# Optimization experiments

Hardware: AMD Instinct MI355X
Metric: run time of the kernel (lower is better)

The kernel has to match this reference:

```python
import jax, jax.numpy as jnp
import numpy as np

LATENT = 256


def setup_inputs() -> dict:
    key = jax.random.key(0)
    ks = jax.random.split(key, 10)
    B, T, V, E, D0, H, L = 512, 200, 3356, 1128, 20000, 1024, LATENT

    def glorot(k, shape):
        fan_out, fan_in = shape
        std = np.sqrt(2.0 / (fan_in + fan_out)).astype(np.float32)
        return jax.random.normal(k, shape, dtype=jnp.float32) * std

    x = jax.random.uniform(ks[0], (B, D0), dtype=jnp.float32)
    item_ids = jax.random.randint(ks[1], (B, T), 0, V, dtype=jnp.int32)
    embed = jax.random.normal(ks[2], (V, E), dtype=jnp.float32)
    Wi = glorot(ks[3], (L, E))
    bi = jnp.zeros((L,), jnp.float32)
    We1 = glorot(ks[4], (H, D0))
    be1 = jnp.zeros((H,), jnp.float32)
    We2 = glorot(ks[5], (2 * L, H))
    be2 = jnp.zeros((2 * L,), jnp.float32)
    Wd1 = glorot(ks[6], (H, L))
    bd1 = jnp.zeros((H,), jnp.float32)
    Wd2 = glorot(ks[7], (D0, H))
    bd2 = jnp.zeros((D0,), jnp.float32)
    # dropout(p=0.5) mask, pre-scaled by 1/(1-p)=2
    drop_mask = (jax.random.bernoulli(ks[8], 0.5, (B, D0))).astype(jnp.float32) * 2.0
    eps = jax.random.normal(ks[9], (B, L), dtype=jnp.float32)
    return {"x": x, "item_ids": item_ids, "embed": embed, "Wi": Wi, "bi": bi,
            "We1": We1, "be1": be1, "We2": We2, "be2": be2,
            "Wd1": Wd1, "bd1": bd1, "Wd2": Wd2, "bd2": bd2,
            "drop_mask": drop_mask, "eps": eps}


def reference(x, item_ids, embed, Wi, bi, We1, be1, We2, be2,
              Wd1, bd1, Wd2, bd2, drop_mask, eps):
    # item feature path: embedding lookup -> linear -> per-sequence stats
    item = jnp.einsum('bte,le->btl', embed[item_ids], Wi) + bi        # [B,T,L]
    mean = jnp.mean(item, axis=1)                                      # [B,L]
    deviation = jnp.std(item, axis=1, ddof=1)                          # torch.std (unbiased)

    # encoder: F.normalize (L2 over features) -> dropout -> tanh MLP
    xn = x / jnp.maximum(jnp.linalg.norm(x, axis=1, keepdims=True), 1e-12)
    h = xn * drop_mask
    h = jnp.tanh(h @ We1.T + be1)
    gparams = h @ We2.T + be2                                          # [B,2L]
    mu, logvar = gparams[:, :LATENT], gparams[:, LATENT:]

    # reparam: MVN with diagonal covariance diag(deviation) == mean + sqrt(dev)*eps
    prior = mean + jnp.sqrt(deviation) * eps
    z = prior * jnp.exp(0.5 * logvar) + mu

    # decoder: tanh MLP
    hd = jnp.tanh(z @ Wd1.T + bd1)
    recon_x = hd @ Wd2.T + bd2                                         # [B,D0]
    return recon_x, mu, logvar
```

## Files before the change

kernel.cpp:

```cpp
#include <hip/hip_runtime.h>
#include <hip/hip_bf16.h>

typedef __bf16 bf16x8 __attribute__((ext_vector_type(8)));
typedef float f32x4 __attribute__((ext_vector_type(4)));
typedef unsigned short u16x8 __attribute__((ext_vector_type(8)));

static __device__ __forceinline__ unsigned short f2bf(float f){
  unsigned int u = __float_as_uint(f);
  u += 0x7fffu + ((u >> 16) & 1u);
  return (unsigned short)(u >> 16);
}

static __device__ __forceinline__ u16x8 cvt8(const float4& a, const float4& b){
  u16x8 r;
  r[0]=f2bf(a.x); r[1]=f2bf(a.y); r[2]=f2bf(a.z); r[3]=f2bf(a.w);
  r[4]=f2bf(b.x); r[5]=f2bf(b.y); r[6]=f2bf(b.z); r[7]=f2bf(b.w);
  return r;
}

static __device__ __forceinline__ void gload16(const void* g, void* l){
  __builtin_amdgcn_global_load_lds(
      (const __attribute__((address_space(1))) unsigned int*)g,
      (__attribute__((address_space(3))) unsigned int*)l, 16, 0, 0);
}

template<int EPI>
__global__ __launch_bounds__(256, 2) void gemm_big(
    const unsigned short* __restrict__ A, const unsigned short* __restrict__ Bw,
    const float* __restrict__ bias,
    float* __restrict__ Cf, unsigned short* __restrict__ Cbf,
    int M, int N, int K, int kchunk)
{
  constexpr int BK = 32;
  constexpr int AE = 128 * BK;
  constexpr int BE = 256 * BK;
  constexpr int BUFE = AE + BE;
  __shared__ unsigned short lds[3 * BUFE];

  const int tid  = threadIdx.x, lane = tid & 63, wave = tid >> 6;
  const int bm0  = blockIdx.y * 128, bn0 = blockIdx.x * 256;
  const int k0   = blockIdx.z * kchunk;
  const int kend = min(K, k0 + kchunk);
  const int nk   = (kend - k0) / BK;
  const int fr = lane & 15, fq = lane >> 4;
  const int wn = wave * 64;

  const int srow = lane >> 2, scol = (lane & 3) * 8;

  auto stage = [&](int buf, int t){
    char* base = (char*)(lds + buf * BUFE);
    const int kk = k0 + t * BK;
    #pragma unroll
    for (int c = 0; c < 2; c++) {
      const int ch = 2 * wave + c;
      const int r = min(bm0 + ch * 16 + srow, M - 1);
      gload16(A + (size_t)r * K + kk + scol, base + ch * 1024);
    }
    #pragma unroll
    for (int c = 0; c < 4; c++) {
      const int ch = 4 * wave + c;
      const int r = min(bn0 + ch * 16 + srow, N - 1);
      gload16(Bw + (size_t)r * K + kk + scol, base + 8192 + ch * 1024);
    }
  };

  stage(0, 0);
  if (nk > 1) stage(1, 1);

  f32x4 acc[8][4] = {};
  int cur = 0;

  for (int t = 0; t < nk; ++t) {
    if (t < nk - 1) asm volatile("s_waitcnt vmcnt(6)" ::: "memory");
    else            asm volatile("s_waitcnt vmcnt(0)" ::: "memory");
    __builtin_amdgcn_s_barrier();
    __builtin_amdgcn_sched_barrier(0);

    if (t + 2 < nk) {
      const int sb = (cur >= 1) ? cur - 1 : cur + 2;
      stage(sb, t + 2);
    }

    const unsigned short* lA = lds + cur * BUFE;
    const unsigned short* lB = lA + AE;
    u16x8 af[8], bg[4];
    #pragma unroll
    for (int i = 0; i < 8; i++) af[i] = *(const u16x8*)&lA[(i*16 + fr) * BK + fq * 8];
    #pragma unroll
    for (int j = 0; j < 4; j++) bg[j] = *(const u16x8*)&lB[(wn + j*16 + fr) * BK + fq * 8];
    #pragma unroll
    for (int j = 0; j < 4; j++)
      #pragma unroll
      for (int i = 0; i < 8; i++)
        acc[i][j] = __builtin_amdgcn_mfma_f32_16x16x32_bf16(
            __builtin_bit_cast(bf16x8, af[i]),
            __builtin_bit_cast(bf16x8, bg[j]),
            acc[i][j], 0, 0, 0);
    asm volatile("s_waitcnt lgkmcnt(0)" ::: "memory");
    __builtin_amdgcn_sched_barrier(0);
    __builtin_amdgcn_s_barrier();
    cur = (cur == 2) ? 0 : cur + 1;
  }

  #pragma unroll
  for (int i = 0; i < 8; i++)
    #pragma unroll
    for (int j = 0; j < 4; j++)
      #pragma unroll
      for (int r = 0; r < 4; r++) {
        int row = bm0 + i*16 + fq*4 + r;
        int col = bn0 + wn + j*16 + fr;
        if (row < M && col < N) {
          float v = acc[i][j][r];
          if constexpr (EPI == 0) {
            Cf[(size_t)row * N + col] = v + (bias ? bias[col] : 0.0f);
          } else if constexpr (EPI == 1) {
            atomicAdd(&Cf[(size_t)row * N + col], v);
          } else {
            Cbf[(size_t)row * N + col] = f2bf(tanhf(v + bias[col]));
          }
        }
      }
}

template<int EPI>
__global__ __launch_bounds__(256) void gemm_sm(
    const unsigned short* __restrict__ A, const unsigned short* __restrict__ Bw,
    const float* __restrict__ bias,
    float* __restrict__ Cf, unsigned short* __restrict__ Cbf,
    int M, int N, int K, int kchunk)
{
  constexpr int BM = 128, BN = 128, BK = 32;
  __shared__ unsigned short lds[(BM + BN) * BK];
  unsigned short* lA = lds;
  unsigned short* lB = lds + BM * BK;

  const int tid  = threadIdx.x, lane = tid & 63, wave = tid >> 6;
  const int bm0  = blockIdx.y * BM, bn0 = blockIdx.x * BN;
  const int k0   = blockIdx.z * kchunk;
  const int kend = min(K, k0 + kchunk);
  const int fr = lane & 15, fq = lane >> 4;
  const int wm = (wave >> 1) * 64, wn = (wave & 1) * 64;

  const bool isA  = wave < 2;
  const int cbase = (wave & 1) * 4;
  const int srow  = lane >> 2, scol = (lane & 3) * 8;
  const unsigned short* G = isA ? A : Bw;
  const int glim = (isA ? M : N) - 1;
  const int g0   = isA ? bm0 : bn0;
  unsigned short* ldst = isA ? lA : lB;

  f32x4 acc[4][4] = {};

  for (int kk = k0; kk < kend; kk += BK) {
    #pragma unroll
    for (int c = 0; c < 4; c++) {
      const int ch = cbase + c;
      const int r = min(g0 + ch * 16 + srow, glim);
      gload16(G + (size_t)r * K + kk + scol, (char*)ldst + ch * 1024);
    }
    __syncthreads();
    u16x8 af[4], bg[4];
    #pragma unroll
    for (int i = 0; i < 4; i++) af[i] = *(const u16x8*)&lA[(wm + i*16 + fr) * BK + fq * 8];
    #pragma unroll
    for (int j = 0; j < 4; j++) bg[j] = *(const u16x8*)&lB[(wn + j*16 + fr) * BK + fq * 8];
    #pragma unroll
    for (int i = 0; i < 4; i++)
      #pragma unroll
      for (int j = 0; j < 4; j++)
        acc[i][j] = __builtin_amdgcn_mfma_f32_16x16x32_bf16(
            __builtin_bit_cast(bf16x8, af[i]),
            __builtin_bit_cast(bf16x8, bg[j]),
            acc[i][j], 0, 0, 0);
    __syncthreads();
  }

  #pragma unroll
  for (int i = 0; i < 4; i++)
    #pragma unroll
    for (int j = 0; j < 4; j++)
      #pragma unroll
      for (int r = 0; r < 4; r++) {
        int row = bm0 + wm + i*16 + fq*4 + r;
        int col = bn0 + wn + j*16 + fr;
        if (row < M && col < N) {
          float v = acc[i][j][r];
          if constexpr (EPI == 0) {
            Cf[(size_t)row * N + col] = v + (bias ? bias[col] : 0.0f);
          } else if constexpr (EPI == 1) {
            atomicAdd(&Cf[(size_t)row * N + col], v);
          } else {
            Cbf[(size_t)row * N + col] = f2bf(tanhf(v + bias[col]));
          }
        }
      }
}

__global__ __launch_bounds__(256) void cvt4_kernel(
    const float* __restrict__ s0, unsigned short* __restrict__ d0, int n0,
    const float* __restrict__ s1, unsigned short* __restrict__ d1, int n1,
    const float* __restrict__ s2, unsigned short* __restrict__ d2, int n2,
    const float* __restrict__ s3, unsigned short* __restrict__ d3, int n3)
{
  int i = (blockIdx.x * 256 + threadIdx.x) * 8;
  const float* s; unsigned short* d;
  if (i < n0)            { s = s0; d = d0; }
  else if ((i -= n0) < n1) { s = s1; d = d1; }
  else if ((i -= n1) < n2) { s = s2; d = d2; }
  else if ((i -= n2) < n3) { s = s3; d = d3; }
  else return;
  const float4* q = (const float4*)(s + i);
  *(u16x8*)(d + i) = cvt8(q[0], q[1]);
}

__global__ __launch_bounds__(256) void cvtpad_kernel(
    const float* __restrict__ src, unsigned short* __restrict__ dst,
    int rows, int scols, int dcols)
{
  int i8 = blockIdx.x * 256 + threadIdx.x;
  int c8 = dcols / 8;
  if (i8 >= rows * c8) return;
  int r = i8 / c8, c0 = (i8 % c8) * 8;
  const float* s = src + (size_t)r * scols;
  u16x8 o;
  #pragma unroll
  for (int e = 0; e < 8; e++) { int c = c0 + e; o[e] = (c < scols) ? f2bf(s[c]) : (unsigned short)0; }
  *(u16x8*)(dst + (size_t)r * dcols + c0) = o;
}

__global__ __launch_bounds__(256) void ynorm_kernel(
    const float* __restrict__ x, const float* __restrict__ dm,
    unsigned short* __restrict__ y, float* __restrict__ ninv, int D0)
{
  const int b = blockIdx.x, tid = threadIdx.x;
  const float4* x4 = (const float4*)(x + (size_t)b * D0);
  const float4* d4 = (const float4*)(dm + (size_t)b * D0);
  ushort4* y4 = (ushort4*)(y + (size_t)b * D0);
  const int n4 = D0 / 4;
  float ss = 0.f;
  for (int i = tid; i < n4; i += 256) {
    float4 xv = x4[i], dv = d4[i];
    ss += xv.x*xv.x + xv.y*xv.y + xv.z*xv.z + xv.w*xv.w;
    ushort4 o;
    o.x = f2bf(xv.x*dv.x); o.y = f2bf(xv.y*dv.y);
    o.z = f2bf(xv.z*dv.z); o.w = f2bf(xv.w*dv.w);
    y4[i] = o;
  }
  #pragma unroll
  for (int off = 32; off > 0; off >>= 1) ss += __shfl_down(ss, off);
  __shared__ float wsum[4];
  if ((tid & 63) == 0) wsum[tid >> 6] = ss;
  __syncthreads();
  if (tid == 0) {
    float t = wsum[0] + wsum[1] + wsum[2] + wsum[3];
    ninv[b] = 1.0f / fmaxf(sqrtf(t), 1e-12f);
  }
}

__global__ __launch_bounds__(256) void stats_kernel(
    const float* __restrict__ proj, const int* __restrict__ ids,
    const float* __restrict__ bi, const float* __restrict__ eps,
    float* __restrict__ prior, int T)
{
  const int b = blockIdx.x, l = threadIdx.x;
  __shared__ int sid[256];
  if (l < T) sid[l] = ids[b * T + l];
  __syncthreads();
  float s1 = 0.f, s2 = 0.f;
  #pragma unroll 4
  for (int t = 0; t < T; t++) {
    float p = proj[(size_t)sid[t] * 256 + l];
    s1 += p; s2 += p * p;
  }
  float var = fmaxf((s2 - s1 * s1 / (float)T) / (float)(T - 1), 0.f);
  float dev = sqrtf(var);
  float mean = s1 / (float)T + bi[l];
  prior[b * 256 + l] = mean + sqrtf(dev) * eps[b * 256 + l];
}

__global__ __launch_bounds__(256) void epi1_kernel(
    const float* __restrict__ C1, const float* __restrict__ ninv,
    const float* __restrict__ be1, unsigned short* __restrict__ h)
{
  int i = blockIdx.x * 256 + threadIdx.x;
  int b = i >> 10, n = i & 1023;
  h[i] = f2bf(tanhf(ninv[b] * C1[i] + be1[n]));
}

__global__ __launch_bounds__(256) void z_kernel(
    const float* __restrict__ gp, const float* __restrict__ prior,
    const float* __restrict__ be2,
    float* __restrict__ out_mu, float* __restrict__ out_lv,
    unsigned short* __restrict__ z)
{
  int i = blockIdx.x * 256 + threadIdx.x;
  int b = i >> 8, l = i & 255;
  float mu = gp[b * 512 + l]       + be2[l];
  float lv = gp[b * 512 + 256 + l] + be2[256 + l];
  out_mu[i] = mu;
  out_lv[i] = lv;
  z[i] = f2bf(prior[i] * expf(0.5f * lv) + mu);
}

extern "C" void kernel_launch(void* const* d_in, const int* in_sizes, int n_in,
                              void* d_out, int out_size, void* d_ws, size_t ws_size,
                              hipStream_t stream)
{
  const float* x     = (const float*)d_in[0];
  const int*   ids   = (const int*)  d_in[1];
  const float* embed = (const float*)d_in[2];
  const float* Wi    = (const float*)d_in[3];
  const float* bi    = (const float*)d_in[4];
  const float* We1   = (const float*)d_in[5];
  const float* be1   = (const float*)d_in[6];
  const float* We2   = (const float*)d_in[7];
  const float* be2   = (const float*)d_in[8];
  const float* Wd1   = (const float*)d_in[9];
  const float* bd1   = (const float*)d_in[10];
  const float* Wd2   = (const float*)d_in[11];
  const float* bd2   = (const float*)d_in[12];
  const float* dm    = (const float*)d_in[13];
  const float* eps   = (const float*)d_in[14];

  constexpr int B = 512, T = 200, V = 3356, E = 1128, Ep = 1152, D0 = 20000, H = 1024, L = 256;

  char* w = (char*)d_ws;
  auto carve = [&](size_t bytes) { char* p = w; w += (bytes + 255) & ~(size_t)255; return p; };
  unsigned short* We1b  = (unsigned short*)carve((size_t)H * D0 * 2);
  unsigned short* Wd2b  = (unsigned short*)carve((size_t)D0 * H * 2);
  unsigned short* We2b  = (unsigned short*)carve((size_t)2 * L * H * 2);
  unsigned short* Wd1b  = (unsigned short*)carve((size_t)H * L * 2);
  unsigned short* embedb= (unsigned short*)carve((size_t)V * Ep * 2);
  unsigned short* Wib   = (unsigned short*)carve((size_t)L * Ep * 2);
  float*          proj  = (float*)         carve((size_t)V * L * 4);
  unsigned short* y     = (unsigned short*)carve((size_t)B * D0 * 2);
  float*          C1    = (float*)         carve((size_t)B * H * 4);
  unsigned short* h     = (unsigned short*)carve((size_t)B * H * 2);
  float*          gp    = (float*)         carve((size_t)B * 2 * L * 4);
  float*          prior = (float*)         carve((size_t)B * L * 4);
  unsigned short* z     = (unsigned short*)carve((size_t)B * L * 2);
  unsigned short* hd    = (unsigned short*)carve((size_t)B * H * 2);
  float*          ninv  = (float*)         carve((size_t)B * 4);

  float* out_recon = (float*)d_out;
  float* out_mu    = out_recon + (size_t)B * D0;
  float* out_lv    = out_mu + (size_t)B * L;

  {
    const int n0 = H * D0, n1 = D0 * H, n2 = 2 * L * H, n3 = H * L;
    const int nblk = (n0 + n1 + n2 + n3) / (8 * 256);
    cvt4_kernel<<<nblk, 256, 0, stream>>>(We1, We1b, n0, Wd2, Wd2b, n1,
                                          We2, We2b, n2, Wd1, Wd1b, n3);
  }
  cvtpad_kernel<<<(V * (Ep/8) + 255) / 256, 256, 0, stream>>>(embed, embedb, V, E, Ep);
  cvtpad_kernel<<<(L * (Ep/8) + 255) / 256, 256, 0, stream>>>(Wi, Wib, L, E, Ep);

  ynorm_kernel<<<B, 256, 0, stream>>>(x, dm, y, ninv, D0);

  hipMemsetAsync(proj, 0, (size_t)V * L * 4, stream);
  gemm_sm<1><<<dim3(2, 27, 4), 256, 0, stream>>>(
      embedb, Wib, nullptr, proj, nullptr, V, L, Ep, 288);
  stats_kernel<<<B, 256, 0, stream>>>(proj, ids, bi, eps, prior, T);

  hipMemsetAsync(C1, 0, (size_t)B * H * 4, stream);
  gemm_big<1><<<dim3(4, 4, 32), 256, 0, stream>>>(
      y, We1b, nullptr, C1, nullptr, B, H, D0, 640);
  epi1_kernel<<<(B * H) / 256, 256, 0, stream>>>(C1, ninv, be1, h);

  hipMemsetAsync(gp, 0, (size_t)B * 2 * L * 4, stream);
  gemm_sm<1><<<dim3(4, 4, 4), 256, 0, stream>>>(
      h, We2b, nullptr, gp, nullptr, B, 2 * L, H, 256);
  z_kernel<<<(B * L) / 256, 256, 0, stream>>>(gp, prior, be2, out_mu, out_lv, z);

  gemm_sm<2><<<dim3(8, 4, 1), 256, 0, stream>>>(
      z, Wd1b, bd1, nullptr, hd, B, H, L, 256);
  gemm_big<0><<<dim3(79, 4, 1), 256, 0, stream>>>(
      hd, Wd2b, bd2, out_recon, nullptr, B, D0, H, 1024);
}
```

Baseline: 296.7 us.

## Read fp32 weights directly in big GEMMs, converting to bf16 in-kernel

The separate pre-conversion pass that turned the two large weight matrices (We1, Wd2) into bf16 copies is removed. The big GEMM now stages fp32 weight tiles into LDS with an XOR swizzle and converts them to bf16 with packed convert instructions before the MFMAs. The tile also shrinks to 128x128 with a 3-deep prefetch, and the grid and split-K are retuned. This cuts a full read and write of about 80MB of weights, but doubles LDS traffic for B and adds conversion ALU work in the inner loop.

```diff
diff --git a/kernel.cpp b/kernel.cpp
--- a/kernel.cpp
+++ b/kernel.cpp
@@ -4,11 +4,18 @@
 typedef __bf16 bf16x8 __attribute__((ext_vector_type(8)));
 typedef float f32x4 __attribute__((ext_vector_type(4)));
 typedef unsigned short u16x8 __attribute__((ext_vector_type(8)));
+typedef unsigned int u32x4 __attribute__((ext_vector_type(4)));
 
 static __device__ __forceinline__ unsigned short f2bf(float f){
   unsigned int u = __float_as_uint(f);
   u += 0x7fffu + ((u >> 16) & 1u);
   return (unsigned short)(u >> 16);
+}
+
+static __device__ __forceinline__ unsigned int cvtpk(float lo, float hi){
+  unsigned int r;
+  asm("v_cvt_pk_bf16_f32 %0, %1, %2" : "=v"(r) : "v"(lo), "v"(hi));
+  return r;
 }
 
 static __device__ __forceinline__ u16x8 cvt8(const float4& a, const float4& b){
@@ -25,146 +32,78 @@
 }
 
 template<int EPI>
-__global__ __launch_bounds__(256, 2) void gemm_big(
-    const unsigned short* __restrict__ A, const unsigned short* __restrict__ Bw,
+__global__ __launch_bounds__(256, 2) void gemm_bigf(
+    const unsigned short* __restrict__ A, const float* __restrict__ Bw,
     const float* __restrict__ bias,
     float* __restrict__ Cf, unsigned short* __restrict__ Cbf,
     int M, int N, int K, int kchunk)
 {
-  constexpr int BK = 32;
-  constexpr int AE = 128 * BK;
-  constexpr int BE = 256 * BK;
-  constexpr int BUFE = AE + BE;
-  __shared__ unsigned short lds[3 * BUFE];
+  constexpr int BK = 32, BUFB = 8192 + 16384;
+  __shared__ char smem[3 * BUFB];
 
   const int tid  = threadIdx.x, lane = tid & 63, wave = tid >> 6;
-  const int bm0  = blockIdx.y * 128, bn0 = blockIdx.x * 256;
+  const int bm0  = blockIdx.y * 128, bn0 = blockIdx.x * 128;
   const int k0   = blockIdx.z * kchunk;
   const int kend = min(K, k0 + kchunk);
   const int nk   = (kend - k0) / BK;
   const int fr = lane & 15, fq = lane >> 4;
-  const int wn = wave * 64;
-
-  const int srow = lane >> 2, scol = (lane & 3) * 8;
+  const int wm = (wave >> 1) * 64, wn = (wave & 1) * 64;
+
+  const int ar_off = wave * 16 + (lane >> 2), ac_off = (lane & 3) * 8;
+  const int br_off = wave * 8 + (lane >> 3);
+  const int bg_off = (((lane & 7) ^ (lane >> 3)) << 2);
 
   auto stage = [&](int buf, int t){
-    char* base = (char*)(lds + buf * BUFE);
+    char* base = smem + buf * BUFB;
     const int kk = k0 + t * BK;
     #pragma unroll
     for (int c = 0; c < 2; c++) {
-      const int ch = 2 * wave + c;
-      const int r = min(bm0 + ch * 16 + srow, M - 1);
-      gload16(A + (size_t)r * K + kk + scol, base + ch * 1024);
+      const int r = min(bm0 + c * 64 + ar_off, M - 1);
+      gload16(A + (size_t)r * K + kk + ac_off, base + c * 4096 + wave * 1024);
     }
     #pragma unroll
     for (int c = 0; c < 4; c++) {
-      const int ch = 4 * wave + c;
-      const int r = min(bn0 + ch * 16 + srow, N - 1);
-      gload16(Bw + (size_t)r * K + kk + scol, base + 8192 + ch * 1024);
+      const int r = min(bn0 + c * 32 + br_off, N - 1);
+      gload16(Bw + (size_t)r * K + kk + bg_off, base + 8192 + c * 4096 + wave * 1024);
     }
   };
 
   stage(0, 0);
   if (nk > 1) stage(1, 1);
-
-  f32x4 acc[8][4] = {};
+  if (nk > 2) stage(2, 2);
+
+  f32x4 acc[4][4] = {};
   int cur = 0;
 
   for (int t = 0; t < nk; ++t) {
-    if (t < nk - 1) asm volatile("s_waitcnt vmcnt(6)" ::: "memory");
-    else            asm volatile("s_waitcnt vmcnt(0)" ::: "memory");
+    const int rem = nk - t - 1;
+    if (rem >= 2)      asm volatile("s_waitcnt vmcnt(12)" ::: "memory");
+    else if (rem == 1) asm volatile("s_waitcnt vmcnt(6)"  ::: "memory");
+    else               asm volatile("s_waitcnt vmcnt(0)"  ::: "memory");
     __builtin_amdgcn_s_barrier();
     __builtin_amdgcn_sched_barrier(0);
 
-    if (t + 2 < nk) {
-      const int sb = (cur >= 1) ? cur - 1 : cur + 2;
-      stage(sb, t + 2);
+    const unsigned short* lA = (const unsigned short*)(smem + cur * BUFB);
+    const char*           lB = smem + cur * BUFB + 8192;
+    u16x8 af[4], bg[4];
+    #pragma unroll
+    for (int i = 0; i < 4; i++) af[i] = *(const u16x8*)&lA[(wm + i*16 + fr) * BK + fq * 8];
+    #pragma unroll
+    for (int j = 0; j < 4; j++) {
+      const int r  = wn + j*16 + fr;
+      const int s0 = (((fq << 1) ^ (r & 7)) << 4);
+      const char* bp = lB + r * 128;
+      f32x4 u = *(const f32x4*)(bp + s0);
+      f32x4 v = *(const f32x4*)(bp + (s0 ^ 16));
+      u32x4 wv; wv[0]=cvtpk(u[0],u[1]); wv[1]=cvtpk(u[2],u[3]);
+                wv[2]=cvtpk(v[0],v[1]); wv[3]=cvtpk(v[2],v[3]);
+      bg[j] = __builtin_bit_cast(u16x8, wv);
     }
-
-    const unsigned short* lA = lds + cur * BUFE;
-    const unsigned short* lB = lA + AE;
-    u16x8 af[8], bg[4];
-    #pragma unroll
-    for (int i = 0; i < 8; i++) af[i] = *(const u16x8*)&lA[(i*16 + fr) * BK + fq * 8];
-    #pragma unroll
-    for (int j = 0; j < 4; j++) bg[j] = *(const u16x8*)&lB[(wn + j*16 + fr) * BK + fq * 8];
-    #pragma unroll
-    for (int j = 0; j < 4; j++)
-      #pragma unroll
-      for (int i = 0; i < 8; i++)
-        acc[i][j] = __builtin_amdgcn_mfma_f32_16x16x32_bf16(
-            __builtin_bit_cast(bf16x8, af[i]),
-            __builtin_bit_cast(bf16x8, bg[j]),
-            acc[i][j], 0, 0, 0);
     asm volatile("s_waitcnt lgkmcnt(0)" ::: "memory");
     __builtin_amdgcn_sched_barrier(0);
     __builtin_amdgcn_s_barrier();
-    cur = (cur == 2) ? 0 : cur + 1;
-  }
-
-  #pragma unroll
-  for (int i = 0; i < 8; i++)
-    #pragma unroll
-    for (int j = 0; j < 4; j++)
-      #pragma unroll
-      for (int r = 0; r < 4; r++) {
-        int row = bm0 + i*16 + fq*4 + r;
-        int col = bn0 + wn + j*16 + fr;
-        if (row < M && col < N) {
-          float v = acc[i][j][r];
-          if constexpr (EPI == 0) {
-            Cf[(size_t)row * N + col] = v + (bias ? bias[col] : 0.0f);
-          } else if constexpr (EPI == 1) {
-            atomicAdd(&Cf[(size_t)row * N + col], v);
-          } else {
-            Cbf[(size_t)row * N + col] = f2bf(tanhf(v + bias[col]));
-          }
-        }
-      }
-}
-
-template<int EPI>
-__global__ __launch_bounds__(256) void gemm_sm(
-    const unsigned short* __restrict__ A, const unsigned short* __restrict__ Bw,
-    const float* __restrict__ bias,
-    float* __restrict__ Cf, unsigned short* __restrict__ Cbf,
-    int M, int N, int K, int kchunk)
-{
-  constexpr int BM = 128, BN = 128, BK = 32;
-  __shared__ unsigned short lds[(BM + BN) * BK];
-  unsigned short* lA = lds;
-  unsigned short* lB = lds + BM * BK;
-
-  const int tid  = threadIdx.x, lane = tid & 63, wave = tid >> 6;
-  const int bm0  = blockIdx.y * BM, bn0 = blockIdx.x * BN;
-  const int k0   = blockIdx.z * kchunk;
-  const int kend = min(K, k0 + kchunk);
-  const int fr = lane & 15, fq = lane >> 4;
-  const int wm = (wave >> 1) * 64, wn = (wave & 1) * 64;
-
-  const bool isA  = wave < 2;
-  const int cbase = (wave & 1) * 4;
-  const int srow  = lane >> 2, scol = (lane & 3) * 8;
-  const unsigned short* G = isA ? A : Bw;
-  const int glim = (isA ? M : N) - 1;
-  const int g0   = isA ? bm0 : bn0;
-  unsigned short* ldst = isA ? lA : lB;
-
-  f32x4 acc[4][4] = {};
-
-  for (int kk = k0; kk < kend; kk += BK) {
-    #pragma unroll
-    for (int c = 0; c < 4; c++) {
-      const int ch = cbase + c;
-      const int r = min(g0 + ch * 16 + srow, glim);
-      gload16(G + (size_t)r * K + kk + scol, (char*)ldst + ch * 1024);
-    }
-    __syncthreads();
-    u16x8 af[4], bg[4];
-    #pragma unroll
-    for (int i = 0; i < 4; i++) af[i] = *(const u16x8*)&lA[(wm + i*16 + fr) * BK + fq * 8];
-    #pragma unroll
-    for (int j = 0; j < 4; j++) bg[j] = *(const u16x8*)&lB[(wn + j*16 + fr) * BK + fq * 8];
+    if (t + 3 < nk) stage(cur, t + 3);
+
     #pragma unroll
     for (int i = 0; i < 4; i++)
       #pragma unroll
@@ -173,7 +112,7 @@
             __builtin_bit_cast(bf16x8, af[i]),
             __builtin_bit_cast(bf16x8, bg[j]),
             acc[i][j], 0, 0, 0);
-    __syncthreads();
+    cur = (cur == 2) ? 0 : cur + 1;
   }
 
   #pragma unroll
@@ -197,6 +136,80 @@
       }
 }
 
+template<int EPI>
+__global__ __launch_bounds__(256) void gemm_sm(
+    const unsigned short* __restrict__ A, const unsigned short* __restrict__ Bw,
+    const float* __restrict__ bias,
+    float* __restrict__ Cf, unsigned short* __restrict__ Cbf,
+    int M, int N, int K, int kchunk)
+{
+  constexpr int BM = 128, BN = 128, BK = 32;
+  __shared__ unsigned short lds[(BM + BN) * BK];
+  unsigned short* lA = lds;
+  unsigned short* lB = lds + BM * BK;
+
+  const int tid  = threadIdx.x, lane = tid & 63, wave = tid >> 6;
+  const int bm0  = blockIdx.y * BM, bn0 = blockIdx.x * BN;
+  const int k0   = blockIdx.z * kchunk;
+  const int kend = min(K, k0 + kchunk);
+  const int fr = lane & 15, fq = lane >> 4;
+  const int wm = (wave >> 1) * 64, wn = (wave & 1) * 64;
+
+  const bool isA  = wave < 2;
+  const int cbase = (wave & 1) * 4;
+  const int srow  = lane >> 2, scol = (lane & 3) * 8;
+  const unsigned short* G = isA ? A : Bw;
+  const int glim = (isA ? M : N) - 1;
+  const int g0   = isA ? bm0 : bn0;
+  unsigned short* ldst = isA ? lA : lB;
+
+  f32x4 acc[4][4] = {};
+
+  for (int kk = k0; kk < kend; kk += BK) {
+    #pragma unroll
+    for (int c = 0; c < 4; c++) {
+      const int ch = cbase + c;
+      const int r = min(g0 + ch * 16 + srow, glim);
+      gload16(G + (size_t)r * K + kk + scol, (char*)ldst + ch * 1024);
+    }
+    __syncthreads();
+    u16x8 af[4], bg[4];
+    #pragma unroll
+    for (int i = 0; i < 4; i++) af[i] = *(const u16x8*)&lA[(wm + i*16 + fr) * BK + fq * 8];
+    #pragma unroll
+    for (int j = 0; j < 4; j++) bg[j] = *(const u16x8*)&lB[(wn + j*16 + fr) * BK + fq * 8];
+    #pragma unroll
+    for (int i = 0; i < 4; i++)
+      #pragma unroll
+      for (int j = 0; j < 4; j++)
+        acc[i][j] = __builtin_amdgcn_mfma_f32_16x16x32_bf16(
+            __builtin_bit_cast(bf16x8, af[i]),
+            __builtin_bit_cast(bf16x8, bg[j]),
+            acc[i][j], 0, 0, 0);
+    __syncthreads();
+  }
+
+  #pragma unroll
+  for (int i = 0; i < 4; i++)
+    #pragma unroll
+    for (int j = 0; j < 4; j++)
+      #pragma unroll
+      for (int r = 0; r < 4; r++) {
+        int row = bm0 + wm + i*16 + fq*4 + r;
+        int col = bn0 + wn + j*16 + fr;
+        if (row < M && col < N) {
+          float v = acc[i][j][r];
+          if constexpr (EPI == 0) {
+            Cf[(size_t)row * N + col] = v + (bias ? bias[col] : 0.0f);
+          } else if constexpr (EPI == 1) {
+            atomicAdd(&Cf[(size_t)row * N + col], v);
+          } else {
+            Cbf[(size_t)row * N + col] = f2bf(tanhf(v + bias[col]));
+          }
+        }
+      }
+}
+
 __global__ __launch_bounds__(256) void cvt4_kernel(
     const float* __restrict__ s0, unsigned short* __restrict__ d0, int n0,
     const float* __restrict__ s1, unsigned short* __restrict__ d1, int n1,
@@ -327,8 +340,6 @@
 
   char* w = (char*)d_ws;
   auto carve = [&](size_t bytes) { char* p = w; w += (bytes + 255) & ~(size_t)255; return p; };
-  unsigned short* We1b  = (unsigned short*)carve((size_t)H * D0 * 2);
-  unsigned short* Wd2b  = (unsigned short*)carve((size_t)D0 * H * 2);
   unsigned short* We2b  = (unsigned short*)carve((size_t)2 * L * H * 2);
   unsigned short* Wd1b  = (unsigned short*)carve((size_t)H * L * 2);
   unsigned short* embedb= (unsigned short*)carve((size_t)V * Ep * 2);
@@ -348,10 +359,9 @@
   float* out_lv    = out_mu + (size_t)B * L;
 
   {
-    const int n0 = H * D0, n1 = D0 * H, n2 = 2 * L * H, n3 = H * L;
-    const int nblk = (n0 + n1 + n2 + n3) / (8 * 256);
-    cvt4_kernel<<<nblk, 256, 0, stream>>>(We1, We1b, n0, Wd2, Wd2b, n1,
-                                          We2, We2b, n2, Wd1, Wd1b, n3);
+    const int n0 = 2 * L * H, n1 = H * L;
+    cvt4_kernel<<<(n0 + n1) / (8 * 256), 256, 0, stream>>>(
+        We2, We2b, n0, Wd1, Wd1b, n1, We2, We2b, 0, We2, We2b, 0);
   }
   cvtpad_kernel<<<(V * (Ep/8) + 255) / 256, 256, 0, stream>>>(embed, embedb, V, E, Ep);
   cvtpad_kernel<<<(L * (Ep/8) + 255) / 256, 256, 0, stream>>>(Wi, Wib, L, E, Ep);
@@ -364,8 +374,8 @@
   stats_kernel<<<B, 256, 0, stream>>>(proj, ids, bi, eps, prior, T);
 
   hipMemsetAsync(C1, 0, (size_t)B * H * 4, stream);
-  gemm_big<1><<<dim3(4, 4, 32), 256, 0, stream>>>(
-      y, We1b, nullptr, C1, nullptr, B, H, D0, 640);
+  gemm_bigf<1><<<dim3(8, 4, 25), 256, 0, stream>>>(
+      y, We1, nullptr, C1, nullptr, B, H, D0, 800);
   epi1_kernel<<<(B * H) / 256, 256, 0, stream>>>(C1, ninv, be1, h);
 
   hipMemsetAsync(gp, 0, (size_t)B * 2 * L * 4, stream);
@@ -375,6 +385,6 @@
 
   gemm_sm<2><<<dim3(8, 4, 1), 256, 0, stream>>>(
       z, Wd1b, bd1, nullptr, hd, B, H, L, 256);
-  gemm_big<0><<<dim3(79, 4, 1), 256, 0, stream>>>(
-      hd, Wd2b, bd2, out_recon, nullptr, B, D0, H, 1024);
-}
+  gemm_bigf<0><<<dim3(157, 4, 1), 256, 0, stream>>>(
+      hd, Wd2, bd2, out_recon, nullptr, B, D0, H, 1024);
+}
```

Result: faster. 287.3 us (-3.2%).

## Replace big GEMM with 256x256-tile, 512-thread, swizzled-LDS double-buffered kernel

Applied to the files above, without the earlier changes.

Replaces the 128x256-tile, 256-thread big GEMM with a 256x256-tile kernel on 512 threads (8 waves in a 2x4 grid). It uses BK=64, double buffering and an XOR-swizzled LDS layout meant to avoid bank conflicts. The next stage's global-to-LDS load is now issued after the fragment reads, so the copy overlaps the MFMA work. The encoder K dimension is zero-padded to 20032 so it divides by 64, which means We1 gets its own padded conversion and the y buffer grows. The larger tile raises data reuse, but the decoder GEMM now launches fewer workgroups with one block per CU, so the GPU may be less filled.

```diff
diff --git a/kernel.cpp b/kernel.cpp
--- a/kernel.cpp
+++ b/kernel.cpp
@@ -25,81 +25,91 @@
 }
 
 template<int EPI>
-__global__ __launch_bounds__(256, 2) void gemm_big(
+__global__ __launch_bounds__(512, 1) void gemm_p2(
     const unsigned short* __restrict__ A, const unsigned short* __restrict__ Bw,
     const float* __restrict__ bias,
     float* __restrict__ Cf, unsigned short* __restrict__ Cbf,
     int M, int N, int K, int kchunk)
 {
-  constexpr int BK = 32;
-  constexpr int AE = 128 * BK;
-  constexpr int BE = 256 * BK;
-  constexpr int BUFE = AE + BE;
-  __shared__ unsigned short lds[3 * BUFE];
-
-  const int tid  = threadIdx.x, lane = tid & 63, wave = tid >> 6;
-  const int bm0  = blockIdx.y * 128, bn0 = blockIdx.x * 256;
-  const int k0   = blockIdx.z * kchunk;
+  constexpr int BK = 64;
+  constexpr int ABYTES = 256 * BK * 2;
+  constexpr int BUFB   = 2 * ABYTES;
+  __shared__ char smem[2 * BUFB];
+
+  const int tid = threadIdx.x, lane = tid & 63, wave = tid >> 6;
+  const int wr = wave >> 2, wc = wave & 3;
+  const int bm0 = blockIdx.y * 256, bn0 = blockIdx.x * 256;
+  const int k0  = blockIdx.z * kchunk;
   const int kend = min(K, k0 + kchunk);
   const int nk   = (kend - k0) / BK;
   const int fr = lane & 15, fq = lane >> 4;
-  const int wn = wave * 64;
-
-  const int srow = lane >> 2, scol = (lane & 3) * 8;
-
-  auto stage = [&](int buf, int t){
-    char* base = (char*)(lds + buf * BUFE);
+
+  const int srow  = lane >> 3;
+  const int scol  = ((lane & 7) ^ (lane >> 3)) * 8;
+
+  auto stage = [&](int t){
+    char* base = smem + (t & 1) * BUFB;
     const int kk = k0 + t * BK;
     #pragma unroll
-    for (int c = 0; c < 2; c++) {
-      const int ch = 2 * wave + c;
-      const int r = min(bm0 + ch * 16 + srow, M - 1);
-      gload16(A + (size_t)r * K + kk + scol, base + ch * 1024);
-    }
-    #pragma unroll
     for (int c = 0; c < 4; c++) {
-      const int ch = 4 * wave + c;
-      const int r = min(bn0 + ch * 16 + srow, N - 1);
-      gload16(Bw + (size_t)r * K + kk + scol, base + 8192 + ch * 1024);
+      const int r = min(bm0 + wave * 32 + c * 8 + srow, M - 1);
+      gload16(A + (size_t)r * K + kk + scol, base + (wave * 4 + c) * 1024);
+    }
+    #pragma unroll
+    for (int c = 0; c < 4; c++) {
+      const int r = min(bn0 + wave * 32 + c * 8 + srow, N - 1);
+      gload16(Bw + (size_t)r * K + kk + scol, base + ABYTES + (wave * 4 + c) * 1024);
     }
   };
 
-  stage(0, 0);
-  if (nk > 1) stage(1, 1);
+  stage(0);
+  if (nk > 1) stage(1);
 
   f32x4 acc[8][4] = {};
-  int cur = 0;
 
   for (int t = 0; t < nk; ++t) {
-    if (t < nk - 1) asm volatile("s_waitcnt vmcnt(6)" ::: "memory");
+    if (t < nk - 1) asm volatile("s_waitcnt vmcnt(8)" ::: "memory");
     else            asm volatile("s_waitcnt vmcnt(0)" ::: "memory");
     __builtin_amdgcn_s_barrier();
     __builtin_amdgcn_sched_barrier(0);
 
-    if (t + 2 < nk) {
-      const int sb = (cur >= 1) ? cur - 1 : cur + 2;
-      stage(sb, t + 2);
-    }
-
-    const unsigned short* lA = lds + cur * BUFE;
-    const unsigned short* lB = lA + AE;
-    u16x8 af[8], bg[4];
-    #pragma unroll
-    for (int i = 0; i < 8; i++) af[i] = *(const u16x8*)&lA[(i*16 + fr) * BK + fq * 8];
-    #pragma unroll
-    for (int j = 0; j < 4; j++) bg[j] = *(const u16x8*)&lB[(wn + j*16 + fr) * BK + fq * 8];
-    #pragma unroll
-    for (int j = 0; j < 4; j++)
-      #pragma unroll
-      for (int i = 0; i < 8; i++)
-        acc[i][j] = __builtin_amdgcn_mfma_f32_16x16x32_bf16(
-            __builtin_bit_cast(bf16x8, af[i]),
-            __builtin_bit_cast(bf16x8, bg[j]),
-            acc[i][j], 0, 0, 0);
+    const char* lA = smem + (t & 1) * BUFB;
+    const char* lB = lA + ABYTES;
+
+    u16x8 af0[8], af1[8], bg0[4], bg1[4];
+    #pragma unroll
+    for (int i = 0; i < 8; i++) {
+      const int r = wr * 128 + i * 16 + fr;
+      const char* rp = lA + r * 128;
+      af0[i] = *(const u16x8*)(rp + ((fq       ^ (r & 7)) << 4));
+      af1[i] = *(const u16x8*)(rp + (((4 + fq) ^ (r & 7)) << 4));
+    }
+    #pragma unroll
+    for (int j = 0; j < 4; j++) {
+      const int r = wc * 64 + j * 16 + fr;
+      const char* rp = lB + r * 128;
+      bg0[j] = *(const u16x8*)(rp + ((fq       ^ (r & 7)) << 4));
+      bg1[j] = *(const u16x8*)(rp + (((4 + fq) ^ (r & 7)) << 4));
+    }
     asm volatile("s_waitcnt lgkmcnt(0)" ::: "memory");
     __builtin_amdgcn_sched_barrier(0);
     __builtin_amdgcn_s_barrier();
-    cur = (cur == 2) ? 0 : cur + 1;
+    if (t + 2 < nk) stage(t + 2);
+
+    #pragma unroll
+    for (int i = 0; i < 8; i++)
+      #pragma unroll
+      for (int j = 0; j < 4; j++)
+        acc[i][j] = __builtin_amdgcn_mfma_f32_16x16x32_bf16(
+            __builtin_bit_cast(bf16x8, af0[i]), __builtin_bit_cast(bf16x8, bg0[j]),
+            acc[i][j], 0, 0, 0);
+    #pragma unroll
+    for (int i = 0; i < 8; i++)
+      #pragma unroll
+      for (int j = 0; j < 4; j++)
+        acc[i][j] = __builtin_amdgcn_mfma_f32_16x16x32_bf16(
+            __builtin_bit_cast(bf16x8, af1[i]), __builtin_bit_cast(bf16x8, bg1[j]),
+            acc[i][j], 0, 0, 0);
   }
 
   #pragma unroll
@@ -108,8 +118,8 @@
     for (int j = 0; j < 4; j++)
       #pragma unroll
       for (int r = 0; r < 4; r++) {
-        int row = bm0 + i*16 + fq*4 + r;
-        int col = bn0 + wn + j*16 + fr;
+        int row = bm0 + wr * 128 + i * 16 + fq * 4 + r;
+        int col = bn0 + wc * 64 + j * 16 + fr;
         if (row < M && col < N) {
           float v = acc[i][j][r];
           if constexpr (EPI == 0) {
@@ -231,20 +241,24 @@
 
 __global__ __launch_bounds__(256) void ynorm_kernel(
     const float* __restrict__ x, const float* __restrict__ dm,
-    unsigned short* __restrict__ y, float* __restrict__ ninv, int D0)
+    unsigned short* __restrict__ y, float* __restrict__ ninv, int D0, int D0p)
 {
   const int b = blockIdx.x, tid = threadIdx.x;
   const float4* x4 = (const float4*)(x + (size_t)b * D0);
   const float4* d4 = (const float4*)(dm + (size_t)b * D0);
-  ushort4* y4 = (ushort4*)(y + (size_t)b * D0);
-  const int n4 = D0 / 4;
+  ushort4* y4 = (ushort4*)(y + (size_t)b * D0p);
+  const int n4 = D0 / 4, n4p = D0p / 4;
   float ss = 0.f;
-  for (int i = tid; i < n4; i += 256) {
-    float4 xv = x4[i], dv = d4[i];
-    ss += xv.x*xv.x + xv.y*xv.y + xv.z*xv.z + xv.w*xv.w;
+  for (int i = tid; i < n4p; i += 256) {
     ushort4 o;
-    o.x = f2bf(xv.x*dv.x); o.y = f2bf(xv.y*dv.y);
-    o.z = f2bf(xv.z*dv.z); o.w = f2bf(xv.w*dv.w);
+    if (i < n4) {
+      float4 xv = x4[i], dv = d4[i];
+      ss += xv.x*xv.x + xv.y*xv.y + xv.z*xv.z + xv.w*xv.w;
+      o.x = f2bf(xv.x*dv.x); o.y = f2bf(xv.y*dv.y);
+      o.z = f2bf(xv.z*dv.z); o.w = f2bf(xv.w*dv.w);
+    } else {
+      o.x = o.y = o.z = o.w = 0;
+    }
     y4[i] = o;
   }
   #pragma unroll
@@ -323,18 +337,19 @@
   const float* dm    = (const float*)d_in[13];
   const float* eps   = (const float*)d_in[14];
 
-  constexpr int B = 512, T = 200, V = 3356, E = 1128, Ep = 1152, D0 = 20000, H = 1024, L = 256;
+  constexpr int B = 512, T = 200, V = 3356, E = 1128, Ep = 1152,
+                D0 = 20000, D0p = 20032, H = 1024, L = 256;
 
   char* w = (char*)d_ws;
   auto carve = [&](size_t bytes) { char* p = w; w += (bytes + 255) & ~(size_t)255; return p; };
-  unsigned short* We1b  = (unsigned short*)carve((size_t)H * D0 * 2);
+  unsigned short* We1b  = (unsigned short*)carve((size_t)H * D0p * 2);
   unsigned short* Wd2b  = (unsigned short*)carve((size_t)D0 * H * 2);
   unsigned short* We2b  = (unsigned short*)carve((size_t)2 * L * H * 2);
   unsigned short* Wd1b  = (unsigned short*)carve((size_t)H * L * 2);
   unsigned short* embedb= (unsigned short*)carve((size_t)V * Ep * 2);
   unsigned short* Wib   = (unsigned short*)carve((size_t)L * Ep * 2);
   float*          proj  = (float*)         carve((size_t)V * L * 4);
-  unsigned short* y     = (unsigned short*)carve((size_t)B * D0 * 2);
+  unsigned short* y     = (unsigned short*)carve((size_t)B * D0p * 2);
   float*          C1    = (float*)         carve((size_t)B * H * 4);
   unsigned short* h     = (unsigned short*)carve((size_t)B * H * 2);
   float*          gp    = (float*)         carve((size_t)B * 2 * L * 4);
@@ -348,15 +363,15 @@
   float* out_lv    = out_mu + (size_t)B * L;
 
   {
-    const int n0 = H * D0, n1 = D0 * H, n2 = 2 * L * H, n3 = H * L;
-    const int nblk = (n0 + n1 + n2 + n3) / (8 * 256);
-    cvt4_kernel<<<nblk, 256, 0, stream>>>(We1, We1b, n0, Wd2, Wd2b, n1,
-                                          We2, We2b, n2, Wd1, Wd1b, n3);
-  }
+    const int n0 = D0 * H, n1 = 2 * L * H, n2 = H * L;
+    cvt4_kernel<<<(n0 + n1 + n2) / (8 * 256), 256, 0, stream>>>(
+        Wd2, Wd2b, n0, We2, We2b, n1, Wd1, Wd1b, n2, Wd1, Wd1b, 0);
+  }
+  cvtpad_kernel<<<(H * (D0p/8) + 255) / 256, 256, 0, stream>>>(We1, We1b, H, D0, D0p);
   cvtpad_kernel<<<(V * (Ep/8) + 255) / 256, 256, 0, stream>>>(embed, embedb, V, E, Ep);
   cvtpad_kernel<<<(L * (Ep/8) + 255) / 256, 256, 0, stream>>>(Wi, Wib, L, E, Ep);
 
-  ynorm_kernel<<<B, 256, 0, stream>>>(x, dm, y, ninv, D0);
+  ynorm_kernel<<<B, 256, 0, stream>>>(x, dm, y, ninv, D0, D0p);
 
   hipMemsetAsync(proj, 0, (size_t)V * L * 4, stream);
   gemm_sm<1><<<dim3(2, 27, 4), 256, 0, stream>>>(
@@ -364,8 +379,8 @@
   stats_kernel<<<B, 256, 0, stream>>>(proj, ids, bi, eps, prior, T);
 
   hipMemsetAsync(C1, 0, (size_t)B * H * 4, stream);
-  gemm_big<1><<<dim3(4, 4, 32), 256, 0, stream>>>(
-      y, We1b, nullptr, C1, nullptr, B, H, D0, 640);
+  gemm_p2<1><<<dim3(4, 2, 32), 512, 0, stream>>>(
+      y, We1b, nullptr, C1, nullptr, B, H, D0p, 640);
   epi1_kernel<<<(B * H) / 256, 256, 0, stream>>>(C1, ninv, be1, h);
 
   hipMemsetAsync(gp, 0, (size_t)B * 2 * L * 4, stream);
@@ -375,6 +390,6 @@
 
   gemm_sm<2><<<dim3(8, 4, 1), 256, 0, stream>>>(
       z, Wd1b, bd1, nullptr, hd, B, H, L, 256);
-  gemm_big<0><<<dim3(79, 4, 1), 256, 0, stream>>>(
+  gemm_p2<0><<<dim3(79, 2, 1), 512, 0, stream>>>(
       hd, Wd2b, bd2, out_recon, nullptr, B, D0, H, 1024);
 }
```

Result: slower. 326.4 us (+10.0%).
